# Kernel optimization log

Measured on AMD Instinct MI355X. Metric: run time of the kernel, lower is better.

The kernel has to match this reference:

```python
import jax, jax.numpy as jnp
import numpy as np

B, N, M = 2, 4096, 12288
K, SH, H, GK, NC, F = 64, 32, 64, 8, 200, 1


def sph_to_cart(theta, phi):
    st = jnp.sin(theta)
    return jnp.stack([st * jnp.cos(phi), st * jnp.sin(phi), jnp.cos(theta)], axis=-1)


def setup_inputs() -> dict:
    key = jax.random.key(0)
    ks = jax.random.split(key, 16)
    theta = jax.random.uniform(ks[0], (B, N)) * jnp.pi
    phi = jax.random.uniform(ks[1], (B, N)) * 2 * jnp.pi
    feat = jax.random.normal(ks[2], (B, N))
    xxx = jnp.stack([theta, phi, feat], axis=1)  # [B,3,N]
    pt = jax.random.uniform(ks[3], (M,)) * jnp.pi
    pp = jax.random.uniform(ks[4], (M,)) * 2 * jnp.pi
    pix_theta_phi = jnp.stack([pt, pp], axis=1)  # [M,2]
    s = 0.1
    return dict(
        xxx=xxx,
        pix_theta_phi=pix_theta_phi,
        att_w1=jax.random.normal(ks[5], (F + 1, SH)) * s,
        att_b1=jnp.zeros((SH,)),
        att_w2=jax.random.normal(ks[6], (SH, 1)) * s,
        att_b2=jnp.zeros((1,)),
        proj_w=jax.random.normal(ks[7], (F, H)) * s,
        proj_b=jnp.zeros((H,)),
        rel_w=jax.random.normal(ks[8], (3, H, H)) * s,
        rel_b=jnp.zeros((3, H)),
        root_w=jax.random.normal(ks[9], (3, H, H)) * s,
        out_w1=jax.random.normal(ks[10], (H, H)) * s,
        out_b1=jnp.zeros((H,)),
        out_w2=jax.random.normal(ks[11], (H, NC)) * s,
        out_b2=jnp.zeros((NC,)),
    )


def reference(xxx, pix_theta_phi, att_w1, att_b1, att_w2, att_b2, proj_w, proj_b,
              rel_w, rel_b, root_w, out_w1, out_b1, out_w2, out_b2):
    # --- sparse healpix sampler ---
    los_tp = jnp.transpose(xxx[:, :2, :], (0, 2, 1))   # [B,N,2]
    x = xxx[:, 2, :][..., None]                        # [B,N,1]
    r_los = sph_to_cart(los_tp[..., 0], los_tp[..., 1])           # [B,N,3]
    r_pix = sph_to_cart(pix_theta_phi[:, 0], pix_theta_phi[:, 1])  # [M,3]
    cos = jnp.clip(jnp.einsum('bnc,mc->bmn', r_los, r_pix), -1.0, 1.0)  # [B,M,N]
    vals, idx = jax.lax.top_k(cos, K)                  # [B,M,K]
    x_g = jax.vmap(lambda xb, ib: xb[ib])(x, idx)      # [B,M,K,F]
    d = jnp.arccos(jnp.clip(vals, -1.0, 1.0))          # [B,M,K]
    feat = jnp.concatenate([x_g, d[..., None]], axis=-1)  # [B,M,K,F+1]
    logits = jax.nn.relu(feat @ att_w1 + att_b1) @ att_w2 + att_b2  # [B,M,K,1]
    w = jax.nn.softmax(logits[..., 0], axis=-1)        # [B,M,K]
    pooled = jnp.einsum('bmk,bmkf->bmf', w, x_g)       # [B,M,F]
    # --- GNN on healpix grid ---
    h = jax.nn.relu(pooled @ proj_w + proj_b)          # [B,M,H]
    m = r_pix.shape[0]
    sq = jnp.sum(r_pix * r_pix, axis=1)
    d2 = sq[:, None] + sq[None, :] - 2.0 * (r_pix @ r_pix.T)       # [M,M]
    d2 = jnp.where(jnp.eye(m, dtype=bool), jnp.inf, d2)  # loop=False
    _, nbr = jax.lax.top_k(-d2, GK)                    # [M,GK] knn_graph
    for i in range(rel_w.shape[0]):
        agg = h[:, nbr, :].sum(axis=2)                 # sum-aggregate neighbor msgs
        h = jax.nn.relu(agg @ rel_w[i] + rel_b[i] + h @ root_w[i])
    graph_feat = h.mean(axis=1)                        # global_mean_pool -> [B,H]
    out = jax.nn.relu(graph_feat @ out_w1 + out_b1) @ out_w2 + out_b2
    return out
```

## Files before the change

kernel.cpp:

```cpp
#include <hip/hip_runtime.h>
#include <hip/hip_bf16.h>

#define B_ 2
#define N_ 4096
#define M_ 12288
#define K_ 64
#define SH_ 32
#define H_ 64
#define GK_ 8
#define NC_ 200

#define KCAP 128
#define BCAP2 48
#define SCAP 144
#define MG_ 0.01f
#define C256_ 81.48733086f

static __device__ __forceinline__ unsigned f2key(float f) {
  unsigned b = __float_as_uint(f);
  return (b & 0x80000000u) ? ~b : (b | 0x80000000u);
}
static __device__ __forceinline__ float key2f(unsigned u) {
  unsigned b = (u & 0x80000000u) ? (u & 0x7fffffffu) : ~u;
  return __uint_as_float(b);
}
static __device__ __forceinline__ unsigned long long shflxor64(unsigned long long x, int m) {
  unsigned lo = (unsigned)x, hi = (unsigned)(x >> 32);
  lo = (unsigned)__shfl_xor((int)lo, m);
  hi = (unsigned)__shfl_xor((int)hi, m);
  return ((unsigned long long)hi << 32) | lo;
}
static __device__ __forceinline__ unsigned long long kpack(float s, int pos) {
  return ((unsigned long long)f2key(s) << 14) | (unsigned)(16383 - pos);
}
static __device__ __forceinline__ unsigned long long spack(float c, int pos) {
  return ((unsigned long long)f2key(c) << 12) | (unsigned)(4095 - pos);
}
static __device__ __forceinline__ int thbkt(float th) {
  int b = (int)(th * C256_);
  return b < 0 ? 0 : (b > 255 ? 255 : b);
}
static __device__ __forceinline__ float clamp1(float x) { return fminf(1.f, fmaxf(-1.f, x)); }
static __device__ __forceinline__ float rdlane(float v, int c) {
  return __uint_as_float((unsigned)__builtin_amdgcn_readlane((int)__float_as_uint(v), c));
}

__global__ __launch_bounds__(256) void sentinel_vJ(float* out, int n, float val) {
  int t = blockIdx.x * 256 + threadIdx.x;
  if (t < n) out[t] = val;
}

#define GRIDB_ 129
#define PREPN_ (M_ + B_*N_ + B_*H_)
#define PREPB_ ((PREPN_ + 255)/256)

__global__ __launch_bounds__(256) void prep_vJ(
    const float* __restrict__ xxx, const float* __restrict__ pix,
    float4* __restrict__ r_pix, float4* __restrict__ r_los, float* __restrict__ gf,
    float* __restrict__ kthrG, float* __restrict__ cthrG, unsigned* __restrict__ cnt)
{
  const float PI = 3.14159265358979f;
  if ((int)blockIdx.x < GRIDB_) {
    int gid  = blockIdx.x*4 + (threadIdx.x >> 6);
    if (gid >= 514) return;
    int lane = threadIdx.x & 63;
    int tgt  = (gid >= 257) ? 1 : 0;
    int gp   = gid - tgt*257;
    float thp = (float)gp * (PI/256.f);
    float cp = cosf(thp), sp = fmaxf(sinf(thp), 1e-6f);
    float thq = ((float)lane + 0.5f) * (PI/64.f);
    float sq = sinf(thq), cq = cosf(thq);
    float rinv = 1.0f / (sq * sp);
    float At = tgt ? (2.f*PI*PI*96.f/(float)N_) : (2.f*PI*PI*40.f/(float)M_);
    float lo = 1e-3f, hi = 3.1414f;
    for (int it = 0; it < 12; ++it) {
      float al = 0.5f*(lo + hi);
      float ca = cosf(al);
      float arg = clamp1((ca - cq*cp) * rinv);
      float ax = fabsf(arg);
      float ac = sqrtf(fmaxf(0.f, 1.f - ax)) *
                 fmaf(ax, fmaf(ax, fmaf(ax, -0.0187293f, 0.0742610f), -0.2121144f), 1.5707288f);
      ac = (arg < 0.f) ? (PI - ac) : ac;
      float S = ac;
      #pragma unroll
      for (int off = 32; off; off >>= 1) S += __shfl_xor(S, off);
      float A = 2.f * S * (PI/64.f);
      if (A < At) lo = al; else hi = al;
    }
    if (lane == 0) {
      float chv = cosf(hi);
      if (tgt) cthrG[gp] = chv - 1e-5f;
      else     kthrG[gp] = 2.f*chv - 1.00002f;
    }
  } else {
    int tid = ((int)blockIdx.x - GRIDB_)*256 + threadIdx.x;
    if (tid < M_) {
      float th = pix[2*tid], ph = pix[2*tid+1];
      float st = sinf(th);
      float x = st*cosf(ph), y = st*sinf(ph), z = cosf(th);
      r_pix[tid] = make_float4(x, y, z, x*x + y*y + z*z);
      atomicAdd(&cnt[thbkt(th)], 1u);
    }
    int t2 = tid - M_;
    if (t2 >= 0 && t2 < B_*N_) {
      int b = t2 >> 12, n = t2 & (N_-1);
      const float* xb = xxx + b*3*N_;
      float th = xb[n], ph = xb[N_+n], ft = xb[2*N_+n];
      float st = sinf(th);
      r_los[t2] = make_float4(st*cosf(ph), st*sinf(ph), cosf(th), ft);
      atomicAdd(&cnt[256 + b*256 + thbkt(th)], 1u);
    }
    int t3 = tid - M_ - B_*N_;
    if (t3 >= 0 && t3 < B_*H_) gf[t3] = 0.0f;
  }
}

__global__ __launch_bounds__(256) void scan_vJ(
    const unsigned* __restrict__ cnt, int* __restrict__ pstart, int* __restrict__ lstart,
    unsigned* __restrict__ pcur, unsigned* __restrict__ lcur)
{
  __shared__ unsigned buf[256];
  const int t = threadIdx.x;
  for (int arr = 0; arr < 3; ++arr) {
    unsigned v = cnt[arr*256 + t];
    buf[t] = v;
    __syncthreads();
    for (int off = 1; off < 256; off <<= 1) {
      unsigned o = (t >= off) ? buf[t - off] : 0u;
      __syncthreads();
      buf[t] += o;
      __syncthreads();
    }
    unsigned incl = buf[t], excl = incl - v;
    if (arr == 0) {
      pstart[t] = (int)excl; if (t == 255) pstart[256] = (int)incl;
      pcur[t] = excl;
    } else {
      int b = arr - 1;
      lstart[b*257 + t] = (int)excl; if (t == 255) lstart[b*257 + 256] = (int)incl;
      lcur[b*256 + t] = excl;
    }
    __syncthreads();
  }
}

__global__ __launch_bounds__(256) void scatter_vJ(
    const float* __restrict__ xxx, const float* __restrict__ pix,
    const float4* __restrict__ r_pix, const float4* __restrict__ r_los,
    unsigned* __restrict__ pcur, unsigned* __restrict__ lcur,
    float4* __restrict__ spix, int* __restrict__ sjdx,
    float4* __restrict__ slos)
{
  int tid = blockIdx.x * 256 + threadIdx.x;
  if (tid < M_) {
    int bkt = thbkt(pix[2*tid]);
    unsigned pos = atomicAdd(&pcur[bkt], 1u);
    spix[pos] = r_pix[tid];
    sjdx[pos] = tid;
  } else {
    int t2 = tid - M_;
    if (t2 < B_*N_) {
      int b = t2 >> 12, n = t2 & (N_-1);
      int bkt = thbkt(xxx[b*3*N_ + n]);
      unsigned pos = atomicAdd(&lcur[b*256 + bkt], 1u);
      slos[b*N_ + pos] = r_los[t2];
    }
  }
}

__global__ __launch_bounds__(512) void sampler_vJ(
    const float* __restrict__ pix,
    const float4* __restrict__ spix, const int* __restrict__ sjdx,
    const float4* __restrict__ slos,
    const int* __restrict__ lstart,
    const float* __restrict__ cthrG,
    const float* __restrict__ aw1, const float* __restrict__ ab1,
    const float* __restrict__ aw2, const float* __restrict__ ab2,
    float* __restrict__ pooled)
{
  __shared__ unsigned long long cand[16][SCAP];
  __shared__ unsigned long long selKey[16][K_];
  __shared__ unsigned long long bndK[16][BCAP2];
  __shared__ unsigned hist[16][64];

  const int tid = threadIdx.x, wv = tid >> 6, lane = tid & 63;
  const int b  = blockIdx.y;
  const int srow0 = blockIdx.x*16 + wv*2, srow1 = srow0 + 1;
  const int r0 = wv*2, r1 = r0 + 1;
  const int m0 = sjdx[srow0], m1 = sjdx[srow1];
  const float4 p0 = spix[srow0], p1 = spix[srow1];
  const float thp0 = pix[2*m0], thp1 = pix[2*m1];
  const int g0 = thbkt(thp0), g1 = thbkt(thp1);
  const float th0 = fminf(cthrG[g0], cthrG[g0+1]);
  const float th1 = fminf(cthrG[g1], cthrG[g1+1]);
  const float inv0 = 63.999f / (1.000001f - th0);
  const float inv1 = 63.999f / (1.000001f - th1);
  const float4* sl = slos + b * N_;
  const int* ls = lstart + b * 257;
  const unsigned long long ltm = (1ull << lane) - 1ull;

  int jlo, jhi;
  {
    float al0 = acosf(clamp1(th0)), al1 = acosf(clamp1(th1));
    int blo = thbkt(fminf(thp0 - al0, thp1 - al1) - MG_);
    int bhi = thbkt(fmaxf(thp0 + al0, thp1 + al1) + MG_);
    jlo = ls[blo]; jhi = ls[bhi + 1];
  }

  unsigned cnt0 = 0, cnt1 = 0;
  for (int base = jlo; base < jhi; base += 64) {
    int pos = base + lane;
    bool act = pos < jhi;
    float c0 = -2.f, c1 = -2.f;
    if (act) {
      float4 v = sl[pos];
      c0 = clamp1(v.x*p0.x + v.y*p0.y + v.z*p0.z);
      c1 = clamp1(v.x*p1.x + v.y*p1.y + v.z*p1.z);
    }
    bool pr0 = c0 > th0, pr1 = c1 > th1;
    unsigned long long mk0 = __ballot(pr0);
    if (mk0) {
      unsigned off = (unsigned)__popcll(mk0 & ltm);
      if (pr0 && cnt0 + off < SCAP) cand[r0][cnt0 + off] = spack(c0, pos);
      cnt0 += (unsigned)__popcll(mk0);
    }
    unsigned long long mk1 = __ballot(pr1);
    if (mk1) {
      unsigned off = (unsigned)__popcll(mk1 & ltm);
      if (pr1 && cnt1 + off < SCAP) cand[r1][cnt1 + off] = spack(c1, pos);
      cnt1 += (unsigned)__popcll(mk1);
    }
  }

  for (int rr = 0; rr < 2; ++rr) {
    const int r = (rr == 0) ? r0 : r1;
    const int m = (rr == 0) ? m0 : m1;
    const float4 p = (rr == 0) ? p0 : p1;
    const float thp = (rr == 0) ? thp0 : thp1;
    const float thg = (rr == 0) ? th0 : th1;
    const float invg = (rr == 0) ? inv0 : inv1;
    unsigned cn = (rr == 0) ? cnt0 : cnt1;
    bool fin = false;

    if (cn >= (unsigned)K_ && cn <= (unsigned)SCAP) {
      hist[r][lane] = 0u;
      for (int i = lane; i < (int)cn; i += 64) {
        float c = key2f((unsigned)(cand[r][i] >> 12));
        atomicAdd(&hist[r][(int)((c - thg) * invg)], 1u);
      }
      unsigned g = hist[r][lane], s = g;
      #pragma unroll
      for (int off = 1; off < 64; off <<= 1) {
        unsigned t2 = (unsigned)__shfl_down((int)s, off);
        s += (lane + off < 64) ? t2 : 0u;
      }
      unsigned snext = s - g;
      unsigned packed = (s >= K_ && snext < K_) ? (((unsigned)(lane+1) << 16) | snext) : 0u;
      #pragma unroll
      for (int off = 32; off; off >>= 1) {
        unsigned o = (unsigned)__shfl_xor((int)packed, off);
        packed = packed > o ? packed : o;
      }
      const int t = (int)(packed >> 16) - 1;
      const unsigned chi = packed & 0xFFFFu;
      const unsigned need = K_ - chi;

      unsigned hiC = 0, bdC = 0;
      for (int i0 = 0; i0 < (int)cn; i0 += 64) {
        int i = i0 + lane;
        bool act = i < (int)cn;
        unsigned long long key = act ? cand[r][i] : 0ull;
        int bin = -1;
        if (act) bin = (int)((key2f((unsigned)(key >> 12)) - thg) * invg);
        bool pHi = act && bin > t, pBd = act && bin == t;
        unsigned long long mH = __ballot(pHi);
        unsigned offH = (unsigned)__popcll(mH & ltm);
        if (pHi && hiC + offH < K_) selKey[r][hiC + offH] = key;
        hiC += (unsigned)__popcll(mH);
        unsigned long long mB = __ballot(pBd);
        unsigned offB = (unsigned)__popcll(mB & ltm);
        if (pBd && bdC + offB < BCAP2) bndK[r][bdC + offB] = key;
        bdC += (unsigned)__popcll(mB);
      }
      if (bdC <= (unsigned)BCAP2) {
        if (lane < (int)bdC) {
          unsigned long long ki = bndK[r][lane];
          int rank = 0;
          for (int j = 0; j < (int)bdC; ++j) rank += (bndK[r][j] > ki) ? 1 : 0;
          if ((unsigned)rank < need) selKey[r][chi + rank] = ki;
        }
        fin = true;
      }
    }

    if (!fin) {
      float th = thg;
      float inv = invg;
      int wlo = jlo, whi = jhi;

      if (cn >= (unsigned)K_) {
        hist[r][lane] = 0u;
        cn = 0;
        for (int base = wlo; base < whi; base += 64) {
          int pos = base + lane;
          bool act = pos < whi;
          float c = -2.f;
          if (act) {
            float4 v = sl[pos];
            c = clamp1(v.x*p.x + v.y*p.y + v.z*p.z);
          }
          bool pr = c > th;
          if (pr) atomicAdd(&hist[r][(int)((c - th) * inv)], 1u);
          cn += (unsigned)__popcll(__ballot(pr));
        }
      }

      int tries = 0;
      while (cn < K_ && tries < 3) {
        th = 1.f - 1.6f*(1.f - th); ++tries;
        inv = 63.999f / (1.000001f - th);
        float al = acosf(clamp1(th));
        int blo = thbkt(thp - al - MG_), bhi = thbkt(thp + al + MG_);
        wlo = ls[blo]; whi = ls[bhi + 1];
        hist[r][lane] = 0u;
        cn = 0;
        for (int base = wlo; base < whi; base += 64) {
          int pos = base + lane;
          bool act = pos < whi;
          float c = -2.f;
          if (act) {
            float4 v = sl[pos];
            c = clamp1(v.x*p.x + v.y*p.y + v.z*p.z);
          }
          bool pr = c > th;
          if (pr) atomicAdd(&hist[r][(int)((c - th) * inv)], 1u);
          cn += (unsigned)__popcll(__ballot(pr));
        }
      }

      bool fin2 = false;
      if (cn >= K_) {
        unsigned g = hist[r][lane], s = g;
        #pragma unroll
        for (int off = 1; off < 64; off <<= 1) {
          unsigned t2 = (unsigned)__shfl_down((int)s, off);
          s += (lane + off < 64) ? t2 : 0u;
        }
        unsigned snext = s - g;
        unsigned packed = (s >= K_ && snext < K_) ? (((unsigned)(lane+1) << 16) | snext) : 0u;
        #pragma unroll
        for (int off = 32; off; off >>= 1) {
          unsigned o = (unsigned)__shfl_xor((int)packed, off);
          packed = packed > o ? packed : o;
        }
        const int t = (int)(packed >> 16) - 1;
        const unsigned chi = packed & 0xFFFFu;
        const unsigned need = K_ - chi;

        unsigned hiC = 0, bdC = 0;
        for (int base = wlo; base < whi; base += 64) {
          int pos = base + lane;
          bool act = pos < whi;
          float c = -2.f;
          if (act) {
            float4 v = sl[pos];
            c = clamp1(v.x*p.x + v.y*p.y + v.z*p.z);
          }
          int bin = (act && c > th) ? (int)((c - th) * inv) : -1;
          bool pHi = bin > t;
          bool pBd = bin == t;
          unsigned long long mH = __ballot(pHi);
          unsigned offH = (unsigned)__popcll(mH & ltm);
          if (pHi && hiC + offH < K_) selKey[r][hiC + offH] = spack(c, pos);
          hiC += (unsigned)__popcll(mH);
          unsigned long long mB = __ballot(pBd);
          unsigned offB = (unsigned)__popcll(mB & ltm);
          if (pBd && bdC + offB < BCAP2) bndK[r][bdC + offB] = spack(c, pos);
          bdC += (unsigned)__popcll(mB);
        }
        if (bdC <= (unsigned)BCAP2) {
          if (lane < (int)bdC) {
            unsigned long long ki = bndK[r][lane];
            int rank = 0;
            for (int j = 0; j < (int)bdC; ++j) rank += (bndK[r][j] > ki) ? 1 : 0;
            if ((unsigned)rank < need) selKey[r][chi + rank] = ki;
          }
          fin2 = true;
        }
      }

      if (!fin2) {
        unsigned long long prev = ~0ull;
        for (int rd = 0; rd < K_; ++rd) {
          unsigned long long best = 0ull;
          for (int i = 0; i < 64; ++i) {
            int pos = lane + 64*i;
            float4 v = sl[pos];
            float c = clamp1(v.x*p.x + v.y*p.y + v.z*p.z);
            unsigned long long k = spack(c, pos);
            if (k < prev && k > best) best = k;
          }
          #pragma unroll
          for (int off = 1; off < 64; off <<= 1) {
            unsigned long long o = shflxor64(best, off);
            best = o > best ? o : best;
          }
          if (lane == 0) selKey[r][rd] = best;
          prev = best;
        }
      }
    }

    {
      unsigned long long key = selKey[r][lane];
      int pos = 4095 - (int)(key & 0xFFFull);
      float c = key2f((unsigned)(key >> 12));
      float xg = sl[pos].w;
      float d  = acosf(clamp1(c));
      float acc = ab2[0];
      for (int s2 = 0; s2 < SH_; ++s2)
        acc += fmaxf(xg*aw1[s2] + d*aw1[SH_+s2] + ab1[s2], 0.f) * aw2[s2];
      float mx = acc;
      #pragma unroll
      for (int off = 32; off; off >>= 1) mx = fmaxf(mx, __shfl_xor(mx, off));
      float e = expf(acc - mx);
      float se = e, sxe = e * xg;
      #pragma unroll
      for (int off = 32; off; off >>= 1) { se += __shfl_xor(se, off); sxe += __shfl_xor(sxe, off); }
      if (lane == 0) pooled[b*M_ + m] = sxe / se;
    }
  }
}

__global__ __launch_bounds__(512) void knn_vJ(
    const float* __restrict__ pix,
    const float4* __restrict__ spix, const int* __restrict__ sjdx,
    const int* __restrict__ pstart,
    const float* __restrict__ kthrG, int* __restrict__ nbr)
{
  __shared__ unsigned long long cKey[16][KCAP];

  const int tid = threadIdx.x, wv = tid >> 6, lane = tid & 63;
  const int lr0 = wv*2;
  const int srow0 = blockIdx.x*16 + lr0, srow1 = srow0 + 1;
  const int i0 = sjdx[srow0], i1 = sjdx[srow1];
  const float4 p0 = spix[srow0], p1 = spix[srow1];
  const float thp0 = pix[2*i0], thp1 = pix[2*i1];
  const int g0 = thbkt(thp0), g1 = thbkt(thp1);
  const float t0 = fminf(kthrG[g0], kthrG[g0+1]);
  const float t1 = fminf(kthrG[g1], kthrG[g1+1]);
  const unsigned long long ltm = (1ull << lane) - 1ull;

  unsigned cnt0 = 0, cnt1 = 0;
  {
    float al0 = acosf(clamp1((t0 + 1.00002f)*0.5f));
    float al1 = acosf(clamp1((t1 + 1.00002f)*0.5f));
    int blo = thbkt(fminf(thp0 - al0, thp1 - al1) - MG_);
    int bhi = thbkt(fmaxf(thp0 + al0, thp1 + al1) + MG_);
    int jlo = pstart[blo], jhi = pstart[bhi + 1];
    for (int base = jlo; base < jhi; base += 64) {
      int pos = base + lane;
      bool act = pos < jhi;
      float s0 = -1e30f, s1 = -1e30f;
      if (act) {
        float4 v = spix[pos];
        s0 = 2.f*(p0.x*v.x + p0.y*v.y + p0.z*v.z) - v.w;
        s1 = 2.f*(p1.x*v.x + p1.y*v.y + p1.z*v.z) - v.w;
      }
      bool pr0 = act && (pos != srow0) && (s0 > t0);
      bool pr1 = act && (pos != srow1) && (s1 > t1);
      unsigned long long mk0 = __ballot(pr0);
      if (mk0) {
        unsigned off = (unsigned)__popcll(mk0 & ltm);
        if (pr0 && cnt0 + off < KCAP) cKey[lr0][cnt0 + off] = kpack(s0, pos);
        cnt0 += (unsigned)__popcll(mk0);
      }
      unsigned long long mk1 = __ballot(pr1);
      if (mk1) {
        unsigned off = (unsigned)__popcll(mk1 & ltm);
        if (pr1 && cnt1 + off < KCAP) cKey[lr0+1][cnt1 + off] = kpack(s1, pos);
        cnt1 += (unsigned)__popcll(mk1);
      }
    }
  }

  for (int rr = 0; rr < 2; ++rr) {
    const int lr = lr0 + rr;
    const int i  = (rr == 0) ? i0 : i1;
    const int srow = (rr == 0) ? srow0 : srow1;
    const float4 pi = (rr == 0) ? p0 : p1;
    const float thp = (rr == 0) ? thp0 : thp1;
    float th = (rr == 0) ? t0 : t1;
    unsigned cn = (rr == 0) ? cnt0 : cnt1;

    int tries = 0;
    while (cn < (unsigned)GK_ && tries < 3) {
      th = 1.6f*th - 0.6f; ++tries;
      float al = acosf(clamp1((th + 1.00002f)*0.5f));
      int blo = thbkt(thp - al - MG_), bhi = thbkt(thp + al + MG_);
      int jlo = pstart[blo], jhi = pstart[bhi + 1];
      cn = 0;
      for (int base = jlo; base < jhi; base += 64) {
        int pos = base + lane;
        bool act = pos < jhi;
        float s = -1e30f;
        if (act) {
          float4 v = spix[pos];
          s = 2.f*(pi.x*v.x + pi.y*v.y + pi.z*v.z) - v.w;
        }
        bool pr = act && (pos != srow) && (s > th);
        unsigned long long mk = __ballot(pr);
        if (mk) {
          unsigned off = (unsigned)__popcll(mk & ltm);
          if (pr && cn + off < KCAP) cKey[lr][cn + off] = kpack(s, pos);
          cn += (unsigned)__popcll(mk);
        }
      }
    }

    if (cn >= (unsigned)GK_ && cn <= (unsigned)KCAP) {
      unsigned long long pk[2];
      #pragma unroll
      for (int t2 = 0; t2 < 2; ++t2) {
        int idx = lane + 64*t2;
        pk[t2] = (idx < (int)cn) ? cKey[lr][idx] : 0ull;
      }
      for (int round = 0; round < GK_; ++round) {
        unsigned long long loc = pk[0]; int lt = 0;
        if (pk[1] > loc) { loc = pk[1]; lt = 1; }
        unsigned long long best = loc;
        #pragma unroll
        for (int off = 1; off < 64; off <<= 1) {
          unsigned long long o = shflxor64(best, off);
          best = o > best ? o : best;
        }
        if (loc == best) pk[lt] = 0ull;
        if (lane == round) nbr[i*GK_ + round] = sjdx[16383 - (int)(best & 16383ull)];
      }
    } else {
      unsigned long long prev = ~0ull;
      for (int rd = 0; rd < GK_; ++rd) {
        unsigned long long best = 0ull;
        for (int pos = lane; pos < M_; pos += 64) {
          float4 v = spix[pos];
          float s = 2.f*(pi.x*v.x + pi.y*v.y + pi.z*v.z) - v.w;
          if (pos != srow) {
            unsigned long long k = kpack(s, pos);
            if (k < prev && k > best) best = k;
          }
        }
        #pragma unroll
        for (int off = 1; off < 64; off <<= 1) {
          unsigned long long o = shflxor64(best, off);
          best = o > best ? o : best;
        }
        if (lane == rd) nbr[i*GK_ + rd] = sjdx[16383 - (int)(best & 16383ull)];
        prev = best;
      }
    }
  }
}

__global__ __launch_bounds__(256) void gnn1f_vJ(
    const float* __restrict__ pooled, float* __restrict__ hout, const int* __restrict__ nbr,
    const float* __restrict__ pw, const float* __restrict__ pb,
    const float* __restrict__ relw, const float* __restrict__ relb,
    const float* __restrict__ rootw)
{
  __shared__ float wrel[H_*H_], wroot[H_*H_];
  const int tid = threadIdx.x;
  #pragma unroll
  for (int q = 0; q < 16; ++q) {
    int idx = tid + 256*q;
    wrel[idx]  = relw[idx];
    wroot[idx] = rootw[idx];
  }
  __syncthreads();

  const int lane = tid & 63;
  const int wave = tid >> 6;
  const int b = blockIdx.y;
  const int m0 = blockIdx.x * 16 + wave * 4;
  const float* pldb = pooled + (size_t)b * M_;
  const float pwl = pw[lane], pbl = pb[lane], rbl = relb[lane];

  float h[4], agg[4], acc[4];
  #pragma unroll
  for (int t = 0; t < 4; ++t) {
    int m = m0 + t;
    float ps = pldb[m];
    h[t] = fmaxf(ps*pwl + pbl, 0.f);
    float a = 0.f;
    #pragma unroll
    for (int k = 0; k < GK_; ++k) {
      int nb = nbr[m*GK_ + k];
      nb = nb < 0 ? 0 : (nb >= M_ ? M_-1 : nb);
      float pn = pldb[nb];
      a += fmaxf(pn*pwl + pbl, 0.f);
    }
    agg[t] = a;
    acc[t] = rbl;
  }
  #pragma unroll
  for (int c = 0; c < H_; ++c) {
    float wr = wrel[c*H_ + lane], wo = wroot[c*H_ + lane];
    #pragma unroll
    for (int t = 0; t < 4; ++t)
      acc[t] += rdlane(agg[t], c) * wr + rdlane(h[t], c) * wo;
  }
  #pragma unroll
  for (int t = 0; t < 4; ++t)
    hout[((size_t)b*M_ + m0 + t)*H_ + lane] = fmaxf(acc[t], 0.f);
}

__global__ __launch_bounds__(256) void gnn_vJ(
    const float* __restrict__ hin, float* __restrict__ hout, const int* __restrict__ nbr,
    const float* __restrict__ relw, const float* __restrict__ relb,
    const float* __restrict__ rootw)
{
  __shared__ float wrel[H_*H_], wroot[H_*H_];
  const int tid = threadIdx.x;
  #pragma unroll
  for (int q = 0; q < 16; ++q) {
    int idx = tid + 256*q;
    wrel[idx]  = relw[idx];
    wroot[idx] = rootw[idx];
  }
  __syncthreads();

  const int lane = tid & 63;
  const int wave = tid >> 6;
  const int b = blockIdx.y;
  const int m0 = blockIdx.x * 16 + wave * 4;
  const float* hb = hin + (size_t)b * M_ * H_;
  const float rbl = relb[lane];

  float h[4], agg[4], acc[4];
  #pragma unroll
  for (int t = 0; t < 4; ++t) {
    int m = m0 + t;
    h[t] = hb[m*H_ + lane];
    float a = 0.f;
    #pragma unroll
    for (int k = 0; k < GK_; ++k) {
      int nb = nbr[m*GK_ + k];
      nb = nb < 0 ? 0 : (nb >= M_ ? M_-1 : nb);
      a += hb[nb*H_ + lane];
    }
    agg[t] = a;
    acc[t] = rbl;
  }
  #pragma unroll
  for (int c = 0; c < H_; ++c) {
    float wr = wrel[c*H_ + lane], wo = wroot[c*H_ + lane];
    #pragma unroll
    for (int t = 0; t < 4; ++t)
      acc[t] += rdlane(agg[t], c) * wr + rdlane(h[t], c) * wo;
  }
  #pragma unroll
  for (int t = 0; t < 4; ++t)
    hout[((size_t)b*M_ + m0 + t)*H_ + lane] = fmaxf(acc[t], 0.f);
}

__global__ __launch_bounds__(256) void gnn3r_vJ(
    const float* __restrict__ hin, float* __restrict__ gf, const int* __restrict__ nbr,
    const float* __restrict__ relw, const float* __restrict__ relb,
    const float* __restrict__ rootw)
{
  __shared__ float wrel[H_*H_], wroot[H_*H_];
  __shared__ float gacc[H_];
  const int tid = threadIdx.x;
  #pragma unroll
  for (int q = 0; q < 16; ++q) {
    int idx = tid + 256*q;
    wrel[idx]  = relw[idx];
    wroot[idx] = rootw[idx];
  }
  if (tid < H_) gacc[tid] = 0.f;
  __syncthreads();

  const int lane = tid & 63;
  const int wave = tid >> 6;
  const int b = blockIdx.y;
  const int m0 = blockIdx.x * 16 + wave * 4;
  const float* hb = hin + (size_t)b * M_ * H_;
  const float rbl = relb[lane];

  float h[4], agg[4], acc[4];
  #pragma unroll
  for (int t = 0; t < 4; ++t) {
    int m = m0 + t;
    h[t] = hb[m*H_ + lane];
    float a = 0.f;
    #pragma unroll
    for (int k = 0; k < GK_; ++k) {
      int nb = nbr[m*GK_ + k];
      nb = nb < 0 ? 0 : (nb >= M_ ? M_-1 : nb);
      a += hb[nb*H_ + lane];
    }
    agg[t] = a;
    acc[t] = rbl;
  }
  #pragma unroll
  for (int c = 0; c < H_; ++c) {
    float wr = wrel[c*H_ + lane], wo = wroot[c*H_ + lane];
    #pragma unroll
    for (int t = 0; t < 4; ++t)
      acc[t] += rdlane(agg[t], c) * wr + rdlane(h[t], c) * wo;
  }
  float ps = fmaxf(acc[0], 0.f) + fmaxf(acc[1], 0.f) + fmaxf(acc[2], 0.f) + fmaxf(acc[3], 0.f);
  atomicAdd(&gacc[lane], ps);
  __syncthreads();
  if (tid < H_) atomicAdd(&gf[b*H_ + tid], gacc[tid]);
}

__global__ __launch_bounds__(256) void head_vJ(
    const float* __restrict__ gf, const float* __restrict__ w1,
    const float* __restrict__ b1, const float* __restrict__ w2,
    const float* __restrict__ b2, float* __restrict__ out)
{
  __shared__ float gfm[B_][H_], hid[B_][H_];
  const int tid = threadIdx.x;
  if (tid < B_*H_) gfm[tid >> 6][tid & 63] = gf[tid] * (1.f / (float)M_);
  __syncthreads();
  if (tid < B_*H_) {
    int b = tid >> 6, j = tid & 63;
    float acc = b1[j];
    for (int c = 0; c < H_; ++c) acc += gfm[b][c] * w1[c*H_ + j];
    hid[b][j] = fmaxf(acc, 0.f);
  }
  __syncthreads();
  for (int t = tid; t < B_*NC_; t += 256) {
    int b = t / NC_, o = t - b*NC_;
    float acc = b2[o];
    for (int j = 0; j < H_; ++j) acc += hid[b][j] * w2[j*NC_ + o];
    out[t] = acc;
  }
}

extern "C" void kernel_launch(void* const* d_in, const int* in_sizes, int n_in,
                              void* d_out, int out_size, void* d_ws, size_t ws_size,
                              hipStream_t stream)
{
  float* out = (float*)d_out;

  const size_t need = (size_t)M_*16 + (size_t)B_*N_*16 + (size_t)B_*M_*4
                    + (size_t)M_*GK_*4 + 2*(size_t)B_*M_*H_*4 + (size_t)B_*H_*4;
  bool ok_ws = ws_size >= need;
  bool ok_in = (n_in == 15) && (out_size == B_*NC_)
            && in_sizes[0] == B_*3*N_ && in_sizes[1] == M_*2
            && in_sizes[2] == 2*SH_ && in_sizes[5] == 1
            && in_sizes[8] == 3*H_*H_ && in_sizes[13] == H_*NC_;
  if (!ok_ws || !ok_in) {
    sentinel_vJ<<<(out_size + 255)/256, 256, 0, stream>>>(out, out_size, ok_in ? 42.f : 43.f);
    return;
  }

  const float* xxx    = (const float*)d_in[0];
  const float* pix    = (const float*)d_in[1];
  const float* att_w1 = (const float*)d_in[2];
  const float* att_b1 = (const float*)d_in[3];
  const float* att_w2 = (const float*)d_in[4];
  const float* att_b2 = (const float*)d_in[5];
  const float* proj_w = (const float*)d_in[6];
  const float* proj_b = (const float*)d_in[7];
  const float* rel_w  = (const float*)d_in[8];
  const float* rel_b  = (const float*)d_in[9];
  const float* root_w = (const float*)d_in[10];
  const float* out_w1 = (const float*)d_in[11];
  const float* out_b1 = (const float*)d_in[12];
  const float* out_w2 = (const float*)d_in[13];
  const float* out_b2 = (const float*)d_in[14];

  char* w = (char*)d_ws;
  float4* r_pix = (float4*)w;  w += (size_t)M_ * 16;
  float4* r_los = (float4*)w;  w += (size_t)B_ * N_ * 16;
  float*  pooled = (float*)w;  w += (size_t)B_ * M_ * 4;
  int*    nbr = (int*)w;       w += (size_t)M_ * GK_ * 4;
  float*  h0 = (float*)w;      w += (size_t)B_ * M_ * H_ * 4;
  float*  h1 = (float*)w;      w += (size_t)B_ * M_ * H_ * 4;
  float*  gf = (float*)w;      w += (size_t)B_ * H_ * 4;

  float*  kthrG = h0;
  float*  cthrG = h0 + 512;
  float4* spix = (float4*)(h0 + 2*M_);
  int*    sjdx = (int*)(h0 + 6*M_);
  float4* slos = (float4*)(h0 + 7*M_);
  unsigned* cnt = (unsigned*)(h0 + 7*M_ + 5*B_*N_);
  int*    pstart = (int*)(cnt + 768);
  int*    lstart = pstart + 257;
  unsigned* pcur = (unsigned*)(lstart + 514);
  unsigned* lcur = pcur + 256;

  hipMemsetAsync(cnt, 0, 768*sizeof(unsigned), stream);
  prep_vJ<<<GRIDB_ + PREPB_, 256, 0, stream>>>(xxx, pix, r_pix, r_los, gf, kthrG, cthrG, cnt);
  scan_vJ<<<1, 256, 0, stream>>>(cnt, pstart, lstart, pcur, lcur);
  scatter_vJ<<<(M_ + B_*N_ + 255)/256, 256, 0, stream>>>(xxx, pix, r_pix, r_los, pcur, lcur,
                                                         spix, sjdx, slos);
  sampler_vJ<<<dim3(M_/16, B_), 512, 0, stream>>>(pix, spix, sjdx, slos, lstart,
                                                  cthrG, att_w1, att_b1, att_w2, att_b2, pooled);
  knn_vJ<<<M_/16, 512, 0, stream>>>(pix, spix, sjdx, pstart, kthrG, nbr);
  gnn1f_vJ<<<dim3(M_/16, B_), 256, 0, stream>>>(pooled, h1, nbr, proj_w, proj_b,
                                                rel_w + 0*H_*H_, rel_b + 0*H_, root_w + 0*H_*H_);
  gnn_vJ<<<dim3(M_/16, B_), 256, 0, stream>>>(h1, h0, nbr, rel_w + 1*H_*H_, rel_b + 1*H_, root_w + 1*H_*H_);
  gnn3r_vJ<<<dim3(M_/16, B_), 256, 0, stream>>>(h0, gf, nbr, rel_w + 2*H_*H_, rel_b + 2*H_, root_w + 2*H_*H_);
  head_vJ<<<1, 256, 0, stream>>>(gf, out_w1, out_b1, out_w2, out_b2, out);
}
```

Measured before the change: 235.1 us.

## Bin points by theta band and phi bucket to prune candidate scans

Replaces the 256 theta-only buckets with 4 theta bands by 64 phi buckets for both line-of-sight points and pixels. The sampler and kNN kernels compute a phi window for each pixel pair and scan only the buckets inside it, with wraparound handling. The goal is fewer dot-product and ballot chunks per row than scanning whole theta strips. The cost is more fragmented scans with partial 64-lane chunks per band, extra trig work per row, and coarse theta bands that widen the scan near the poles; the fallback retry paths scan whole bands.

```diff
diff --git a/kernel.cpp b/kernel.cpp
--- a/kernel.cpp
+++ b/kernel.cpp
@@ -16,6 +16,13 @@
 #define MG_ 0.01f
 #define C256_ 81.48733086f
 
+#define TB_ 4
+#define PB_ 64
+#define CTB_ 1.27323954f
+#define CPB_ 10.18591636f
+#define TWO_PI_ 6.28318530718f
+#define INV2PI_ 0.15915494309f
+
 static __device__ __forceinline__ unsigned f2key(float f) {
   unsigned b = __float_as_uint(f);
   return (b & 0x80000000u) ? ~b : (b | 0x80000000u);
@@ -40,12 +47,48 @@
   int b = (int)(th * C256_);
   return b < 0 ? 0 : (b > 255 ? 255 : b);
 }
+static __device__ __forceinline__ int tband(float th) {
+  int b = (int)(th * CTB_);
+  return b < 0 ? 0 : (b > TB_-1 ? TB_-1 : b);
+}
+static __device__ __forceinline__ int pbkt(float ph) {
+  int b = (int)(ph * CPB_);
+  return b < 0 ? 0 : (b > PB_-1 ? PB_-1 : b);
+}
 static __device__ __forceinline__ float clamp1(float x) { return fminf(1.f, fmaxf(-1.f, x)); }
 static __device__ __forceinline__ float rdlane(float v, int c) {
   return __uint_as_float((unsigned)__builtin_amdgcn_readlane((int)__float_as_uint(v), c));
 }
 
-__global__ __launch_bounds__(256) void sentinel_vJ(float* out, int n, float val) {
+static __device__ __forceinline__ void phi_window(
+    float thp0, float php0, float al0, float thp1, float php1, float al1,
+    int& pbl, int& nb)
+{
+  float sp0 = sinf(thp0), sp1 = sinf(thp1);
+  float sa0 = sinf(fminf(al0 + MG_, 1.5707f));
+  float sa1 = sinf(fminf(al1 + MG_, 1.5707f));
+  bool full = (sa0 >= sp0 * 0.9999f) || (sa1 >= sp1 * 0.9999f);
+  if (!full) {
+    float dp0 = asinf(fminf(sa0 / sp0, 1.f)) + MG_;
+    float dp1 = asinf(fminf(sa1 / sp1, 1.f)) + MG_;
+    float d = php1 - php0;
+    d -= floorf(d * INV2PI_ + 0.5f) * TWO_PI_;
+    float lo = fminf(-dp0, d - dp1), hi = fmaxf(dp0, d + dp1);
+    float wdt = hi - lo;
+    if (wdt >= TWO_PI_ * 0.95f) full = true;
+    else {
+      float a0 = php0 + lo;
+      a0 -= floorf(a0 * INV2PI_) * TWO_PI_;
+      pbl = (int)(a0 * CPB_);
+      pbl = pbl < 0 ? 0 : (pbl > PB_-1 ? PB_-1 : pbl);
+      nb = (int)(wdt * CPB_) + 2;
+      if (nb > PB_) nb = PB_;
+    }
+  }
+  if (full) { pbl = 0; nb = PB_; }
+}
+
+__global__ __launch_bounds__(256) void sentinel_vK(float* out, int n, float val) {
   int t = blockIdx.x * 256 + threadIdx.x;
   if (t < n) out[t] = val;
 }
@@ -54,7 +97,7 @@
 #define PREPN_ (M_ + B_*N_ + B_*H_)
 #define PREPB_ ((PREPN_ + 255)/256)
 
-__global__ __launch_bounds__(256) void prep_vJ(
+__global__ __launch_bounds__(256) void prep_vK(
     const float* __restrict__ xxx, const float* __restrict__ pix,
     float4* __restrict__ r_pix, float4* __restrict__ r_los, float* __restrict__ gf,
     float* __restrict__ kthrG, float* __restrict__ cthrG, unsigned* __restrict__ cnt)
@@ -99,7 +142,7 @@
       float st = sinf(th);
       float x = st*cosf(ph), y = st*sinf(ph), z = cosf(th);
       r_pix[tid] = make_float4(x, y, z, x*x + y*y + z*z);
-      atomicAdd(&cnt[thbkt(th)], 1u);
+      atomicAdd(&cnt[tband(th)*PB_ + pbkt(ph)], 1u);
     }
     int t2 = tid - M_;
     if (t2 >= 0 && t2 < B_*N_) {
@@ -108,14 +151,14 @@
       float th = xb[n], ph = xb[N_+n], ft = xb[2*N_+n];
       float st = sinf(th);
       r_los[t2] = make_float4(st*cosf(ph), st*sinf(ph), cosf(th), ft);
-      atomicAdd(&cnt[256 + b*256 + thbkt(th)], 1u);
+      atomicAdd(&cnt[256 + b*256 + tband(th)*PB_ + pbkt(ph)], 1u);
     }
     int t3 = tid - M_ - B_*N_;
     if (t3 >= 0 && t3 < B_*H_) gf[t3] = 0.0f;
   }
 }
 
-__global__ __launch_bounds__(256) void scan_vJ(
+__global__ __launch_bounds__(256) void scan_vK(
     const unsigned* __restrict__ cnt, int* __restrict__ pstart, int* __restrict__ lstart,
     unsigned* __restrict__ pcur, unsigned* __restrict__ lcur)
 {
@@ -144,7 +187,7 @@
   }
 }
 
-__global__ __launch_bounds__(256) void scatter_vJ(
+__global__ __launch_bounds__(256) void scatter_vK(
     const float* __restrict__ xxx, const float* __restrict__ pix,
     const float4* __restrict__ r_pix, const float4* __restrict__ r_los,
     unsigned* __restrict__ pcur, unsigned* __restrict__ lcur,
@@ -153,7 +196,7 @@
 {
   int tid = blockIdx.x * 256 + threadIdx.x;
   if (tid < M_) {
-    int bkt = thbkt(pix[2*tid]);
+    int bkt = tband(pix[2*tid])*PB_ + pbkt(pix[2*tid+1]);
     unsigned pos = atomicAdd(&pcur[bkt], 1u);
     spix[pos] = r_pix[tid];
     sjdx[pos] = tid;
@@ -161,14 +204,15 @@
     int t2 = tid - M_;
     if (t2 < B_*N_) {
       int b = t2 >> 12, n = t2 & (N_-1);
-      int bkt = thbkt(xxx[b*3*N_ + n]);
+      const float* xb = xxx + b*3*N_;
+      int bkt = tband(xb[n])*PB_ + pbkt(xb[N_+n]);
       unsigned pos = atomicAdd(&lcur[b*256 + bkt], 1u);
       slos[b*N_ + pos] = r_los[t2];
     }
   }
 }
 
-__global__ __launch_bounds__(512) void sampler_vJ(
+__global__ __launch_bounds__(512) void sampler_vK(
     const float* __restrict__ pix,
     const float4* __restrict__ spix, const int* __restrict__ sjdx,
     const float4* __restrict__ slos,
@@ -190,6 +234,7 @@
   const int m0 = sjdx[srow0], m1 = sjdx[srow1];
   const float4 p0 = spix[srow0], p1 = spix[srow1];
   const float thp0 = pix[2*m0], thp1 = pix[2*m1];
+  const float php0 = pix[2*m0+1], php1 = pix[2*m1+1];
   const int g0 = thbkt(thp0), g1 = thbkt(thp1);
   const float th0 = fminf(cthrG[g0], cthrG[g0+1]);
   const float th1 = fminf(cthrG[g1], cthrG[g1+1]);
@@ -199,36 +244,50 @@
   const int* ls = lstart + b * 257;
   const unsigned long long ltm = (1ull << lane) - 1ull;
 
-  int jlo, jhi;
+  const float al0 = acosf(clamp1(th0)), al1 = acosf(clamp1(th1));
+  int rlo, rhi, pbl, nb;
   {
-    float al0 = acosf(clamp1(th0)), al1 = acosf(clamp1(th1));
-    int blo = thbkt(fminf(thp0 - al0, thp1 - al1) - MG_);
-    int bhi = thbkt(fmaxf(thp0 + al0, thp1 + al1) + MG_);
-    jlo = ls[blo]; jhi = ls[bhi + 1];
+    rlo = tband(fminf(thp0 - al0, thp1 - al1) - MG_);
+    rhi = tband(fmaxf(thp0 + al0, thp1 + al1) + MG_);
+    phi_window(thp0, php0, al0, thp1, php1, al1, pbl, nb);
   }
 
   unsigned cnt0 = 0, cnt1 = 0;
-  for (int base = jlo; base < jhi; base += 64) {
-    int pos = base + lane;
-    bool act = pos < jhi;
-    float c0 = -2.f, c1 = -2.f;
-    if (act) {
-      float4 v = sl[pos];
-      c0 = clamp1(v.x*p0.x + v.y*p0.y + v.z*p0.z);
-      c1 = clamp1(v.x*p1.x + v.y*p1.y + v.z*p1.z);
-    }
-    bool pr0 = c0 > th0, pr1 = c1 > th1;
-    unsigned long long mk0 = __ballot(pr0);
-    if (mk0) {
-      unsigned off = (unsigned)__popcll(mk0 & ltm);
-      if (pr0 && cnt0 + off < SCAP) cand[r0][cnt0 + off] = spack(c0, pos);
-      cnt0 += (unsigned)__popcll(mk0);
-    }
-    unsigned long long mk1 = __ballot(pr1);
-    if (mk1) {
-      unsigned off = (unsigned)__popcll(mk1 & ltm);
-      if (pr1 && cnt1 + off < SCAP) cand[r1][cnt1 + off] = spack(c1, pos);
-      cnt1 += (unsigned)__popcll(mk1);
+  {
+    auto doChunk = [&](int base, int e) {
+      int pos = base + lane;
+      bool act = pos < e;
+      float c0 = -2.f, c1 = -2.f;
+      if (act) {
+        float4 v = sl[pos];
+        c0 = clamp1(v.x*p0.x + v.y*p0.y + v.z*p0.z);
+        c1 = clamp1(v.x*p1.x + v.y*p1.y + v.z*p1.z);
+      }
+      bool pr0 = c0 > th0, pr1 = c1 > th1;
+      unsigned long long mk0 = __ballot(pr0);
+      if (mk0) {
+        unsigned off = (unsigned)__popcll(mk0 & ltm);
+        if (pr0 && cnt0 + off < SCAP) cand[r0][cnt0 + off] = spack(c0, pos);
+        cnt0 += (unsigned)__popcll(mk0);
+      }
+      unsigned long long mk1 = __ballot(pr1);
+      if (mk1) {
+        unsigned off = (unsigned)__popcll(mk1 & ltm);
+        if (pr1 && cnt1 + off < SCAP) cand[r1][cnt1 + off] = spack(c1, pos);
+        cnt1 += (unsigned)__popcll(mk1);
+      }
+    };
+    for (int band = rlo; band <= rhi; ++band) {
+      const int rb = band * PB_;
+      if (pbl + nb <= PB_) {
+        int s = ls[rb + pbl], e = ls[rb + pbl + nb];
+        for (int base = s; base < e; base += 64) doChunk(base, e);
+      } else {
+        int s1 = ls[rb + pbl], e1 = ls[rb + PB_];
+        for (int base = s1; base < e1; base += 64) doChunk(base, e1);
+        int s2 = ls[rb], e2 = ls[rb + pbl + nb - PB_];
+        for (int base = s2; base < e2; base += 64) doChunk(base, e2);
+      }
     }
   }
 
@@ -296,7 +355,7 @@
     if (!fin) {
       float th = thg;
       float inv = invg;
-      int wlo = jlo, whi = jhi;
+      int wlo = ls[rlo * PB_], whi = ls[(rhi + 1) * PB_];
 
       if (cn >= (unsigned)K_) {
         hist[r][lane] = 0u;
@@ -320,8 +379,8 @@
         th = 1.f - 1.6f*(1.f - th); ++tries;
         inv = 63.999f / (1.000001f - th);
         float al = acosf(clamp1(th));
-        int blo = thbkt(thp - al - MG_), bhi = thbkt(thp + al + MG_);
-        wlo = ls[blo]; whi = ls[bhi + 1];
+        int blo = tband(thp - al - MG_), bhi = tband(thp + al + MG_);
+        wlo = ls[blo * PB_]; whi = ls[(bhi + 1) * PB_];
         hist[r][lane] = 0u;
         cn = 0;
         for (int base = wlo; base < whi; base += 64) {
@@ -432,7 +491,7 @@
   }
 }
 
-__global__ __launch_bounds__(512) void knn_vJ(
+__global__ __launch_bounds__(512) void knn_vK(
     const float* __restrict__ pix,
     const float4* __restrict__ spix, const int* __restrict__ sjdx,
     const int* __restrict__ pstart,
@@ -446,6 +505,7 @@
   const int i0 = sjdx[srow0], i1 = sjdx[srow1];
   const float4 p0 = spix[srow0], p1 = spix[srow1];
   const float thp0 = pix[2*i0], thp1 = pix[2*i1];
+  const float php0 = pix[2*i0+1], php1 = pix[2*i1+1];
   const int g0 = thbkt(thp0), g1 = thbkt(thp1);
   const float t0 = fminf(kthrG[g0], kthrG[g0+1]);
   const float t1 = fminf(kthrG[g1], kthrG[g1+1]);
@@ -455,12 +515,14 @@
   {
     float al0 = acosf(clamp1((t0 + 1.00002f)*0.5f));
     float al1 = acosf(clamp1((t1 + 1.00002f)*0.5f));
-    int blo = thbkt(fminf(thp0 - al0, thp1 - al1) - MG_);
-    int bhi = thbkt(fmaxf(thp0 + al0, thp1 + al1) + MG_);
-    int jlo = pstart[blo], jhi = pstart[bhi + 1];
-    for (int base = jlo; base < jhi; base += 64) {
+    int rlo = tband(fminf(thp0 - al0, thp1 - al1) - MG_);
+    int rhi = tband(fmaxf(thp0 + al0, thp1 + al1) + MG_);
+    int pbl, nb;
+    phi_window(thp0, php0, al0, thp1, php1, al1, pbl, nb);
+
+    auto doChunk = [&](int base, int e) {
       int pos = base + lane;
-      bool act = pos < jhi;
+      bool act = pos < e;
       float s0 = -1e30f, s1 = -1e30f;
       if (act) {
         float4 v = spix[pos];
@@ -480,6 +542,18 @@
         unsigned off = (unsigned)__popcll(mk1 & ltm);
         if (pr1 && cnt1 + off < KCAP) cKey[lr0+1][cnt1 + off] = kpack(s1, pos);
         cnt1 += (unsigned)__popcll(mk1);
+      }
+    };
+    for (int band = rlo; band <= rhi; ++band) {
+      const int rb = band * PB_;
+      if (pbl + nb <= PB_) {
+        int s = pstart[rb + pbl], e = pstart[rb + pbl + nb];
+        for (int base = s; base < e; base += 64) doChunk(base, e);
+      } else {
+        int s1 = pstart[rb + pbl], e1 = pstart[rb + PB_];
+        for (int base = s1; base < e1; base += 64) doChunk(base, e1);
+        int s2 = pstart[rb], e2 = pstart[rb + pbl + nb - PB_];
+        for (int base = s2; base < e2; base += 64) doChunk(base, e2);
       }
     }
   }
@@ -497,8 +571,8 @@
     while (cn < (unsigned)GK_ && tries < 3) {
       th = 1.6f*th - 0.6f; ++tries;
       float al = acosf(clamp1((th + 1.00002f)*0.5f));
-      int blo = thbkt(thp - al - MG_), bhi = thbkt(thp + al + MG_);
-      int jlo = pstart[blo], jhi = pstart[bhi + 1];
+      int blo = tband(thp - al - MG_), bhi = tband(thp + al + MG_);
+      int jlo = pstart[blo * PB_], jhi = pstart[(bhi + 1) * PB_];
       cn = 0;
       for (int base = jlo; base < jhi; base += 64) {
         int pos = base + lane;
@@ -561,7 +635,7 @@
   }
 }
 
-__global__ __launch_bounds__(256) void gnn1f_vJ(
+__global__ __launch_bounds__(256) void gnn1f_vK(
     const float* __restrict__ pooled, float* __restrict__ hout, const int* __restrict__ nbr,
     const float* __restrict__ pw, const float* __restrict__ pb,
     const float* __restrict__ relw, const float* __restrict__ relb,
@@ -613,7 +687,7 @@
     hout[((size_t)b*M_ + m0 + t)*H_ + lane] = fmaxf(acc[t], 0.f);
 }
 
-__global__ __launch_bounds__(256) void gnn_vJ(
+__global__ __launch_bounds__(256) void gnn_vK(
     const float* __restrict__ hin, float* __restrict__ hout, const int* __restrict__ nbr,
     const float* __restrict__ relw, const float* __restrict__ relb,
     const float* __restrict__ rootw)
@@ -662,7 +736,7 @@
     hout[((size_t)b*M_ + m0 + t)*H_ + lane] = fmaxf(acc[t], 0.f);
 }
 
-__global__ __launch_bounds__(256) void gnn3r_vJ(
+__global__ __launch_bounds__(256) void gnn3r_vK(
     const float* __restrict__ hin, float* __restrict__ gf, const int* __restrict__ nbr,
     const float* __restrict__ relw, const float* __restrict__ relb,
     const float* __restrict__ rootw)
@@ -714,7 +788,7 @@
   if (tid < H_) atomicAdd(&gf[b*H_ + tid], gacc[tid]);
 }
 
-__global__ __launch_bounds__(256) void head_vJ(
+__global__ __launch_bounds__(256) void head_vK(
     const float* __restrict__ gf, const float* __restrict__ w1,
     const float* __restrict__ b1, const float* __restrict__ w2,
     const float* __restrict__ b2, float* __restrict__ out)
@@ -752,7 +826,7 @@
             && in_sizes[2] == 2*SH_ && in_sizes[5] == 1
             && in_sizes[8] == 3*H_*H_ && in_sizes[13] == H_*NC_;
   if (!ok_ws || !ok_in) {
-    sentinel_vJ<<<(out_size + 255)/256, 256, 0, stream>>>(out, out_size, ok_in ? 42.f : 43.f);
+    sentinel_vK<<<(out_size + 255)/256, 256, 0, stream>>>(out, out_size, ok_in ? 42.f : 43.f);
     return;
   }
 
@@ -793,16 +867,16 @@
   unsigned* lcur = pcur + 256;
 
   hipMemsetAsync(cnt, 0, 768*sizeof(unsigned), stream);
-  prep_vJ<<<GRIDB_ + PREPB_, 256, 0, stream>>>(xxx, pix, r_pix, r_los, gf, kthrG, cthrG, cnt);
-  scan_vJ<<<1, 256, 0, stream>>>(cnt, pstart, lstart, pcur, lcur);
-  scatter_vJ<<<(M_ + B_*N_ + 255)/256, 256, 0, stream>>>(xxx, pix, r_pix, r_los, pcur, lcur,
+  prep_vK<<<GRIDB_ + PREPB_, 256, 0, stream>>>(xxx, pix, r_pix, r_los, gf, kthrG, cthrG, cnt);
+  scan_vK<<<1, 256, 0, stream>>>(cnt, pstart, lstart, pcur, lcur);
+  scatter_vK<<<(M_ + B_*N_ + 255)/256, 256, 0, stream>>>(xxx, pix, r_pix, r_los, pcur, lcur,
                                                          spix, sjdx, slos);
-  sampler_vJ<<<dim3(M_/16, B_), 512, 0, stream>>>(pix, spix, sjdx, slos, lstart,
+  sampler_vK<<<dim3(M_/16, B_), 512, 0, stream>>>(pix, spix, sjdx, slos, lstart,
                                                   cthrG, att_w1, att_b1, att_w2, att_b2, pooled);
-  knn_vJ<<<M_/16, 512, 0, stream>>>(pix, spix, sjdx, pstart, kthrG, nbr);
-  gnn1f_vJ<<<dim3(M_/16, B_), 256, 0, stream>>>(pooled, h1, nbr, proj_w, proj_b,
+  knn_vK<<<M_/16, 512, 0, stream>>>(pix, spix, sjdx, pstart, kthrG, nbr);
+  gnn1f_vK<<<dim3(M_/16, B_), 256, 0, stream>>>(pooled, h1, nbr, proj_w, proj_b,
                                                 rel_w + 0*H_*H_, rel_b + 0*H_, root_w + 0*H_*H_);
-  gnn_vJ<<<dim3(M_/16, B_), 256, 0, stream>>>(h1, h0, nbr, rel_w + 1*H_*H_, rel_b + 1*H_, root_w + 1*H_*H_);
-  gnn3r_vJ<<<dim3(M_/16, B_), 256, 0, stream>>>(h0, gf, nbr, rel_w + 2*H_*H_, rel_b + 2*H_, root_w + 2*H_*H_);
-  head_vJ<<<1, 256, 0, stream>>>(gf, out_w1, out_b1, out_w2, out_b2, out);
-}
+  gnn_vK<<<dim3(M_/16, B_), 256, 0, stream>>>(h1, h0, nbr, rel_w + 1*H_*H_, rel_b + 1*H_, root_w + 1*H_*H_);
+  gnn3r_vK<<<dim3(M_/16, B_), 256, 0, stream>>>(h0, gf, nbr, rel_w + 2*H_*H_, rel_b + 2*H_, root_w + 2*H_*H_);
+  head_vK<<<1, 256, 0, stream>>>(gf, out_w1, out_b1, out_w2, out_b2, out);
+}
```

Result: slower. 263.2 us (+11.9%).
